# Kernel optimization log

Measured on AMD Instinct MI355X. Metric: run time of the kernel, lower is better.

Reference implementation:

```python
import jax, jax.numpy as jnp
import numpy as np

N_QUBITS = 12
N_LAYERS = 4
BATCH = 4096
DIM = 2 ** N_QUBITS  # 4096


def _apply_1q(state, U, q):
    """Apply 2x2 complex gate U to qubit q. state: (B,) + (2,)*n, wire 0 = MSB (axis q+1)."""
    state = jnp.moveaxis(state, q + 1, -1)
    state = state @ U.T
    return jnp.moveaxis(state, -1, q + 1)


def _apply_cnot(state, c, t):
    """CNOT with control c, target t: flip target amplitudes where control bit == 1."""
    flipped = jnp.flip(state, axis=t + 1)
    shape = [2 if i == c + 1 else 1 for i in range(state.ndim)]
    ctrl = jnp.arange(2).reshape(shape)
    return jnp.where(ctrl == 1, flipped, state)


def setup_inputs() -> dict:
    key = jax.random.key(0)
    k1, k2 = jax.random.split(key)
    x = jax.random.normal(k1, (BATCH, DIM), dtype=jnp.float32)
    weights = jax.random.normal(k2, (N_LAYERS, N_QUBITS, 2), dtype=jnp.float32) * 0.1
    return {"x": x, "weights": weights}


def reference(x, weights):
    n, L = N_QUBITS, N_LAYERS
    B = x.shape[0]
    # AmplitudeEmbedding with normalize=True
    norm = jnp.linalg.norm(x, axis=-1, keepdims=True)
    state = (x / norm).astype(jnp.complex64).reshape((B,) + (2,) * n)
    for layer in range(L):
        for q in range(n):
            ty = weights[layer, q, 0]
            tz = weights[layer, q, 1]
            c, s = jnp.cos(ty / 2), jnp.sin(ty / 2)
            em = jnp.exp(-0.5j * tz.astype(jnp.complex64))  # e^{-i tz/2}
            ep = jnp.exp(+0.5j * tz.astype(jnp.complex64))
            # U = RZ(tz) @ RY(ty), fused single 2x2 gate per qubit
            U = jnp.stack([
                jnp.stack([c * em, -s * em]),
                jnp.stack([s * ep, c * ep]),
            ]).astype(jnp.complex64)
            state = _apply_1q(state, U, q)
        for q in range(n - 1):
            state = _apply_cnot(state, q, q + 1)
        if n > 2:
            state = _apply_cnot(state, n - 1, 0)
    probs = jnp.abs(state) ** 2  # (B,) + (2,)*n, float32
    reduce_axes = tuple(range(1, probs.ndim))
    outs = []
    for q in range(n):
        shape = [2 if i == q + 1 else 1 for i in range(probs.ndim)]
        sign = jnp.array([1.0, -1.0], dtype=probs.dtype).reshape(shape)
        outs.append(jnp.sum(probs * sign, axis=reduce_axes))
    return jnp.stack(outs, axis=-1)  # (B, n_qubits) <Z_q> expvals
```

## Files before the change

### kernel.cpp

```cpp
#include <hip/hip_runtime.h>

#define NQ   12
#define DIM  4096
#define NL   4
#define BLK  256

typedef unsigned short u16;
typedef unsigned int   u32;
typedef float f2 __attribute__((ext_vector_type(2)));

struct L12 { u16 b[NQ]; };

static constexpr u32 lap(const L12& A, u32 x){ u32 r=0; for(int p=0;p<NQ;++p) if((x>>p)&1u) r^=A.b[p]; return r; }
static constexpr L12 lcomp(const L12& A, const L12& B){ L12 r{}; for(int p=0;p<NQ;++p) r.b[p]=(u16)lap(A,(u32)B.b[p]); return r; }
static constexpr L12 lident(){ L12 r{}; for(int p=0;p<NQ;++p) r.b[p]=(u16)(1u<<p); return r; }

static constexpr u32 applyT(u32 i){
  i ^= ((i>>0)&1u) << 11;
  for(int q=10;q>=0;--q){ int pc=11-q, pt=10-q; i ^= ((i>>pc)&1u) << pt; }
  return i;
}
static constexpr L12 lT(){ L12 t{}; for(int p=0;p<NQ;++p) t.b[p]=(u16)applyT(1u<<p); return t; }

static constexpr L12 linv(const L12& A){
  u16 v[NQ]; u16 u[NQ];
  for(int p=0;p<NQ;++p){ v[p]=A.b[p]; u[p]=(u16)(1u<<p); }
  for(int t=0;t<NQ;++t){
    int p=t; while(!((v[p]>>t)&1u)) ++p;
    u16 tv=v[p]; v[p]=v[t]; v[t]=tv; u16 tu=u[p]; u[p]=u[t]; u[t]=tu;
    for(int k=0;k<NQ;++k) if(k!=t && ((v[k]>>t)&1u)){ v[k]^=v[t]; u[k]^=u[t]; }
  }
  L12 r{}; for(int p=0;p<NQ;++p) r.b[p]=u[p]; return r;
}
static constexpr L12 ltr(const L12& A){
  L12 r{}; for(int p=0;p<NQ;++p) for(int q=0;q<NQ;++q) if((A.b[p]>>q)&1u) r.b[q]=(u16)(r.b[q]|(1u<<p));
  return r;
}
static constexpr int cpop(u32 v){ int n=0; while(v){ n+=(int)(v&1u); v>>=1; } return n; }

struct Tables {
  u16 cm[12][16];
  u16 wg[12][4];
  u16 sp[12][4];
  u16 wexp[NQ];
};

static constexpr Tables make_tables(){
  Tables tb{};
  const L12 T   = lT();
  const L12 Tit = ltr(linv(T));
  L12 A = lident();
  L12 W = lident();
  for(int l=0;l<NL;++l){
    for(int g=0;g<3;++g){
      const int st = l*3+g;
      u16 mm[4]={0,0,0,0};
      for(int i=0;i<4;++i){ mm[i]=A.b[4*g+i]; tb.wg[st][i]=W.b[4*g+i]; }
      u32 ech[4]={0,0,0,0}; int piv[4]={0,0,0,0};
      for(int i=0;i<4;++i){
        u32 v=mm[i];
        for(int k=0;k<i;++k) if((v>>piv[k])&1u) v^=ech[k];
        int t2=11; while(!((v>>t2)&1u)) --t2;
        piv[i]=t2; ech[i]=v;
      }
      for(int a2=0;a2<4;++a2) for(int b2=a2+1;b2<4;++b2)
        if(piv[b2]<piv[a2]){ int tt=piv[a2]; piv[a2]=piv[b2]; piv[b2]=tt; }
      for(int i=0;i<4;++i) tb.sp[st][i]=(u16)piv[i];
      for(int c=0;c<16;++c){ u32 m=0; for(int i=0;i<4;++i) if((c>>i)&1) m^=mm[i]; tb.cm[st][c]=(u16)m; }
    }
    A = lcomp(A, T);
    W = lcomp(W, Tit);
  }
  for(int p=0;p<NQ;++p) tb.wexp[p]=W.b[p];
  return tb;
}

__device__ constexpr Tables TB = make_tables();

static constexpr u16 UIMG[12] = {1,2,4,8, 3,5,6,7, 9,10,11,13};

static constexpr u32 swz(u32 j){
  u32 f=0;
  for(int k=4;k<12;++k) if((j>>k)&1u) f ^= (u32)UIMG[k];
  return j ^ (f & 15u);
}

struct Derived {
  u32 lane_c[12][8];
  u32 smb[12][4];
  u32 scmb[12][16];
  u32 g0lane[8];
  u32 u11lane[8];
  u32 u11smb[4];
  u16 pm[12];
  u16 mu[12];
};

static constexpr Derived make_derived(){
  const Tables tb = make_tables();
  Derived d{};
  for(int st=0; st<12; ++st){
    bool isp[12]={false,false,false,false,false,false,false,false,false,false,false,false};
    for(int i=0;i<4;++i) isp[tb.sp[st][i]]=true;
    int np[8]; int nn=0;
    for(int p=0;p<12;++p) if(!isp[p]) np[nn++]=p;
    int best=-1;
    for(int ms=0; ms<256; ++ms){
      int pc=0; for(int k=0;k<8;++k) pc+=(ms>>k)&1;
      if(pc!=6) continue;
      u16 bas[4]={0,0,0,0}; int r=0;
      for(int k=0;k<8;++k){
        if(!((ms>>k)&1)) continue;
        u16 x=(u16)(UIMG[np[k]]&15);
        while(x){
          int hb=3; while(!((x>>hb)&1)) --hb;
          if(bas[hb]) x=(u16)(x^bas[hb]);
          else { bas[hb]=x; ++r; x=0; }
        }
      }
      if(r==4){ best=ms; break; }
    }
    if(best<0) best=0x3F;
    int pos[8]; int lo=0, hi=6;
    for(int k=0;k<8;++k){ if((best>>k)&1) pos[lo++]=np[k]; else pos[hi++]=np[k]; }
    for(int k=0;k<8;++k){
      const u32 addr = swz(1u<<pos[k])<<3;
      u32 nib=0;
      for(int i=0;i<4;++i) nib |= (u32)((tb.wg[st][i]>>pos[k])&1u)<<i;
      d.lane_c[st][k] = addr | (nib<<28);
      if(st==0)  d.g0lane[k]  = 1u<<pos[k];
      if(st==11) d.u11lane[k] = 1u<<pos[k];
    }
    for(int i=0;i<4;++i)  d.smb[st][i]  = swz((u32)tb.cm[st][1<<i])<<3;
    for(int c=0;c<16;++c) d.scmb[st][c] = swz((u32)tb.cm[st][c])<<3;
    if(st==11) for(int i=0;i<4;++i) d.u11smb[i] = (u32)tb.cm[11][1<<i];
  }
  for(int q=0;q<12;++q){
    d.pm[q] = tb.wexp[11-q];
    u32 m=0;
    for(int i=0;i<4;++i) m |= (u32)(cpop((u32)tb.cm[11][1u<<i] & (u32)tb.wexp[11-q])&1)<<i;
    d.mu[q]=(u16)m;
  }
  return d;
}

__device__ constexpr Derived DV = make_derived();

template<int ST, bool WITHW>
__device__ __forceinline__ void gates(f2 (&a)[16], const float4* __restrict__ gw){
#pragma unroll
  for(int i=0;i<4;++i){
    const float4 g = gw[ST*4+i];
    const f2 mt = {-g.x, -g.x};
    const f2 sy = { g.y,  g.y};
#pragma unroll
    for(int c=0;c<16;++c){
      if((c>>i)&1) continue;
      const int c1 = c|(1<<i);
      f2 u = __builtin_elementwise_fma(mt, a[c1], a[c]);
      f2 v = __builtin_elementwise_fma(sy, u, a[c1]);
      a[c] = __builtin_elementwise_fma(mt, v, u);
      if(WITHW){
        const float t = fmaf(-g.z, v.y, v.x);
        v.y = fmaf( g.w, t, v.y);
        v.x = fmaf(-g.z, v.y, t);
      }
      a[c1]=v;
    }
  }
}

template<int ST, bool WITHW>
__device__ __forceinline__ void mid_step(const u32* msk, char* lds, const float4* __restrict__ gw){
  u32 acc=0;
#pragma unroll
  for(int k=0;k<8;++k) acc ^= DV.lane_c[ST][k]&msk[k];
  const u32 nib = acc>>28;
  u32 base = acc & 0x0FFFFFFFu;
#pragma unroll
  for(int i=0;i<4;++i) base ^= DV.smb[ST][i] & (0u-((nib>>i)&1u));
  u32 ad[16]; f2 a[16];
#pragma unroll
  for(int c=0;c<16;++c){
    ad[c] = base ^ DV.scmb[ST][c];
    a[c] = *(const f2*)(lds+ad[c]);
  }
  gates<ST,WITHW>(a,gw);
#pragma unroll
  for(int c=0;c<16;++c){ *(f2*)(lds+ad[c]) = a[c]; }
  __syncthreads();
}

__global__ void prep_kernel(const float* __restrict__ w, float4* __restrict__ gw){
  const int t = threadIdx.x;
  if(t < NL*NQ){
    const int l=t/NQ, p=t%NQ, q=(NQ-1)-p;
    const float ty=w[(l*NQ+q)*2+0], tz=w[(l*NQ+q)*2+1];
    gw[t]=make_float4(tanf(0.25f*ty), sinf(0.5f*ty), tanf(0.5f*tz), sinf(tz));
  }
}

__global__ __launch_bounds__(BLK, 5) void qsim_kernel(const float* __restrict__ x,
                                                      const float4* __restrict__ gw,
                                                      float* __restrict__ out)
{
  __shared__ f2 st2[DIM];
  char* lds = (char*)st2;
  const int tid = threadIdx.x;
  const int bb  = blockIdx.x;

  u32 msk[8];
#pragma unroll
  for(int k=0;k<8;++k) msk[k]=0u-((u32)(tid>>k)&1u);

  u32 rep0=0, acc0=0;
#pragma unroll
  for(int k=0;k<8;++k){ rep0 ^= DV.g0lane[k]&msk[k]; acc0 ^= DV.lane_c[0][k]&msk[k]; }
  const u32 base0 = acc0 & 0x0FFFFFFFu;

  f2 a[16];
  const float* xr = x + (size_t)bb*DIM + rep0;
#pragma unroll
  for(int s=0;s<4;++s){
    const float4 v = *reinterpret_cast<const float4*>(xr + 4*s);
    a[4*s+0]=(f2){v.x,0.f}; a[4*s+1]=(f2){v.y,0.f};
    a[4*s+2]=(f2){v.z,0.f}; a[4*s+3]=(f2){v.w,0.f};
  }
  gates<0,true>(a,gw);
#pragma unroll
  for(int c=0;c<16;++c){ *(f2*)(lds + (base0 ^ DV.scmb[0][c])) = a[c]; }
  __syncthreads();

  mid_step<1,true >(msk,lds,gw);
  mid_step<2,true >(msk,lds,gw);
  mid_step<3,true >(msk,lds,gw);
  mid_step<4,true >(msk,lds,gw);
  mid_step<5,true >(msk,lds,gw);
  mid_step<6,true >(msk,lds,gw);
  mid_step<7,true >(msk,lds,gw);
  mid_step<8,true >(msk,lds,gw);
  mid_step<9,false>(msk,lds,gw);
  mid_step<10,false>(msk,lds,gw);

  {
    u32 acc=0, urep=0;
#pragma unroll
    for(int k=0;k<8;++k){ acc ^= DV.lane_c[11][k]&msk[k]; urep ^= DV.u11lane[k]&msk[k]; }
    const u32 nib = acc>>28;
    u32 base = acc & 0x0FFFFFFFu;
#pragma unroll
    for(int i=0;i<4;++i){ const u32 mi=0u-((nib>>i)&1u); base ^= DV.smb[11][i]&mi; urep ^= DV.u11smb[i]&mi; }
#pragma unroll
    for(int c=0;c<16;++c){
      a[c] = *(const f2*)(lds + (base ^ DV.scmb[11][c]));
    }
    gates<11,false>(a,gw);

    float pr[16];
#pragma unroll
    for(int c=0;c<16;++c) pr[c]=fmaf(a[c].x,a[c].x, a[c].y*a[c].y);
#pragma unroll
    for(int b=1;b<16;b<<=1){
#pragma unroll
      for(int c=0;c<16;++c){
        if(c&b) continue;
        const float u=pr[c], v=pr[c|b];
        pr[c]=u+v; pr[c|b]=u-v;
      }
    }
    float accq[12];
#pragma unroll
    for(int q=0;q<12;++q){
      const u32 sb = ((u32)__popc(urep & (u32)DV.pm[q]) & 1u)<<31;
      accq[q]=__uint_as_float(__float_as_uint(pr[DV.mu[q]])^sb);
    }
    float nrm2 = pr[0];
#pragma unroll
    for(int o=32;o;o>>=1){
      nrm2 += __shfl_xor(nrm2,o);
#pragma unroll
      for(int q=0;q<12;++q) accq[q]+=__shfl_xor(accq[q],o);
    }
    __syncthreads();
    float* wredf = (float*)lds;
    const int wid=tid>>6;
    if((tid&63)==0){
#pragma unroll
      for(int q=0;q<12;++q) wredf[wid*13+q]=accq[q];
      wredf[wid*13+12]=nrm2;
    }
    __syncthreads();
    if(tid<NQ){
      const float s0=wredf[0*13+tid]+wredf[1*13+tid]+wredf[2*13+tid]+wredf[3*13+tid];
      const float sn=wredf[0*13+12]+wredf[1*13+12]+wredf[2*13+12]+wredf[3*13+12];
      out[(size_t)bb*NQ+tid]=s0/sn;
    }
  }
}

extern "C" void kernel_launch(void* const* d_in, const int* in_sizes, int n_in,
                              void* d_out, int out_size, void* d_ws, size_t ws_size,
                              hipStream_t stream) {
  const float* x = (const float*)d_in[0];
  const float* w = (const float*)d_in[1];
  float* out = (float*)d_out;
  float4* gw = (float4*)d_ws;
  const int B = in_sizes[0] / DIM;
  prep_kernel<<<1, 64, 0, stream>>>(w, gw);
  qsim_kernel<<<B, BLK, 0, stream>>>(x, gw, out);
}
```

Measured before the change: 107.0 us.

## Process two batch rows per block with split real/imag packed-FMA layout

Each block now simulates two batch samples at once, storing amplitudes as (re0,re1,im0,im1) float4 in LDS so v_pk_fma_f32 runs on the same component of both samples. This changes the gate arithmetic from mixed real/imag pairs to fully packed operations, doubles the LDS footprint per block, and rebuilds the swizzle/bank selection search for 16-byte entries. Occupancy hint drops from 5 to 2 blocks, and half as many blocks are launched. The aim is to use packed FP32 throughput fully and halve per-sample index/sync overhead, at the cost of more registers and LDS per block.

```diff
diff --git a/kernel.cpp b/kernel.cpp
--- a/kernel.cpp
+++ b/kernel.cpp
@@ -8,6 +8,7 @@
 typedef unsigned short u16;
 typedef unsigned int   u32;
 typedef float f2 __attribute__((ext_vector_type(2)));
+typedef float f4v __attribute__((ext_vector_type(4)));
 
 struct L12 { u16 b[NQ]; };
 
@@ -75,14 +76,24 @@
   return tb;
 }
 
-__device__ constexpr Tables TB = make_tables();
-
 static constexpr u16 UIMG[12] = {1,2,4,8, 3,5,6,7, 9,10,11,13};
 
 static constexpr u32 swz(u32 j){
   u32 f=0;
   for(int k=4;k<12;++k) if((j>>k)&1u) f ^= (u32)UIMG[k];
   return j ^ (f & 15u);
+}
+
+static constexpr int rankbits(const u16* v, int n, u16 mask){
+  u16 bas[4]={0,0,0,0}; int r=0;
+  for(int i=0;i<n;++i){
+    u16 x=(u16)(v[i]&mask);
+    for(int it=0; it<5 && x; ++it){
+      int hb=3; while(hb>0 && !((x>>hb)&1u)) --hb;
+      if(bas[hb]) x=(u16)(x^bas[hb]); else { bas[hb]=x; ++r; x=0; }
+    }
+  }
+  return r;
 }
 
 struct Derived {
@@ -104,35 +115,40 @@
     for(int i=0;i<4;++i) isp[tb.sp[st][i]]=true;
     int np[8]; int nn=0;
     for(int p=0;p<12;++p) if(!isp[p]) np[nn++]=p;
-    int best=-1;
-    for(int ms=0; ms<256; ++ms){
-      int pc=0; for(int k=0;k<8;++k) pc+=(ms>>k)&1;
-      if(pc!=6) continue;
-      u16 bas[4]={0,0,0,0}; int r=0;
-      for(int k=0;k<8;++k){
-        if(!((ms>>k)&1)) continue;
-        u16 x=(u16)(UIMG[np[k]]&15);
-        while(x){
-          int hb=3; while(!((x>>hb)&1)) --hb;
-          if(bas[hb]) x=(u16)(x^bas[hb]);
-          else { bas[hb]=x; ++r; x=0; }
+    u16 img8[8];
+    for(int j=0;j<8;++j) img8[j]=(u16)(swz(1u<<np[j])&15u);
+    int ord[8]={0,1,2,3,4,5,6,7}; bool okf=false;
+    for(int a=0;a<8&&!okf;++a)for(int b=a+1;b<8&&!okf;++b)
+    for(int c2=b+1;c2<8&&!okf;++c2)for(int dd=c2+1;dd<8&&!okf;++dd){
+      u16 four[4]={img8[a],img8[b],img8[c2],img8[dd]};
+      if(rankbits(four,4,15)!=4) continue;
+      const int ids[4]={a,b,c2,dd};
+      for(int ex=0; ex<4 && !okf; ++ex){
+        u16 tri[3]; int tj=0;
+        for(int j=0;j<4;++j) if(j!=ex) tri[tj++]=four[j];
+        if(rankbits(tri,3,7)!=3) continue;
+        int pp=0;
+        for(int j=0;j<4;++j) if(j!=ex) ord[pp++]=ids[j];
+        ord[3]=ids[ex];
+        int rp=4;
+        for(int j=0;j<8;++j){
+          bool used=false; for(int k2=0;k2<4;++k2) if(ids[k2]==j) used=true;
+          if(!used) ord[rp++]=j;
         }
-      }
-      if(r==4){ best=ms; break; }
-    }
-    if(best<0) best=0x3F;
-    int pos[8]; int lo=0, hi=6;
-    for(int k=0;k<8;++k){ if((best>>k)&1) pos[lo++]=np[k]; else pos[hi++]=np[k]; }
+        okf=true;
+      }
+    }
     for(int k=0;k<8;++k){
-      const u32 addr = swz(1u<<pos[k])<<3;
+      const int pos = np[ord[k]];
+      const u32 addr = swz(1u<<pos)<<4;
       u32 nib=0;
-      for(int i=0;i<4;++i) nib |= (u32)((tb.wg[st][i]>>pos[k])&1u)<<i;
+      for(int i=0;i<4;++i) nib |= (u32)((tb.wg[st][i]>>pos)&1u)<<i;
       d.lane_c[st][k] = addr | (nib<<28);
-      if(st==0)  d.g0lane[k]  = 1u<<pos[k];
-      if(st==11) d.u11lane[k] = 1u<<pos[k];
-    }
-    for(int i=0;i<4;++i)  d.smb[st][i]  = swz((u32)tb.cm[st][1<<i])<<3;
-    for(int c=0;c<16;++c) d.scmb[st][c] = swz((u32)tb.cm[st][c])<<3;
+      if(st==0)  d.g0lane[k]  = 1u<<pos;
+      if(st==11) d.u11lane[k] = 1u<<pos;
+    }
+    for(int i=0;i<4;++i)  d.smb[st][i]  = swz((u32)tb.cm[st][1<<i])<<4;
+    for(int c=0;c<16;++c) d.scmb[st][c] = swz((u32)tb.cm[st][c])<<4;
     if(st==11) for(int i=0;i<4;++i) d.u11smb[i] = (u32)tb.cm[11][1<<i];
   }
   for(int q=0;q<12;++q){
@@ -146,26 +162,37 @@
 
 __device__ constexpr Derived DV = make_derived();
 
+__device__ __forceinline__ f2 pkfma(f2 a, f2 b, f2 c){
+  f2 d;
+  asm("v_pk_fma_f32 %0, %1, %2, %3" : "=v"(d) : "v"(a), "v"(b), "v"(c));
+  return d;
+}
+
 template<int ST, bool WITHW>
-__device__ __forceinline__ void gates(f2 (&a)[16], const float4* __restrict__ gw){
+__device__ __forceinline__ void gates(f2 (&R)[16], f2 (&I)[16], const float4* __restrict__ gw){
 #pragma unroll
   for(int i=0;i<4;++i){
     const float4 g = gw[ST*4+i];
-    const f2 mt = {-g.x, -g.x};
-    const f2 sy = { g.y,  g.y};
+    const f2 mt  = {g.x, g.x};
+    const f2 sy  = {g.y, g.y};
+    const f2 mgz = {g.z, g.z};
+    const f2 sw  = {g.w, g.w};
 #pragma unroll
     for(int c=0;c<16;++c){
       if((c>>i)&1) continue;
       const int c1 = c|(1<<i);
-      f2 u = __builtin_elementwise_fma(mt, a[c1], a[c]);
-      f2 v = __builtin_elementwise_fma(sy, u, a[c1]);
-      a[c] = __builtin_elementwise_fma(mt, v, u);
+      f2 uR = pkfma(mt, R[c1], R[c]);
+      f2 uI = pkfma(mt, I[c1], I[c]);
+      f2 vR = pkfma(sy, uR, R[c1]);
+      f2 vI = pkfma(sy, uI, I[c1]);
+      R[c] = pkfma(mt, vR, uR);
+      I[c] = pkfma(mt, vI, uI);
       if(WITHW){
-        const float t = fmaf(-g.z, v.y, v.x);
-        v.y = fmaf( g.w, t, v.y);
-        v.x = fmaf(-g.z, v.y, t);
-      }
-      a[c1]=v;
+        const f2 tr = pkfma(mgz, vI, vR);
+        vI = pkfma(sw, tr, vI);
+        vR = pkfma(mgz, vI, tr);
+      }
+      R[c1]=vR; I[c1]=vI;
     }
   }
 }
@@ -179,15 +206,16 @@
   u32 base = acc & 0x0FFFFFFFu;
 #pragma unroll
   for(int i=0;i<4;++i) base ^= DV.smb[ST][i] & (0u-((nib>>i)&1u));
-  u32 ad[16]; f2 a[16];
+  u32 ad[16]; f2 R[16], I[16];
 #pragma unroll
   for(int c=0;c<16;++c){
     ad[c] = base ^ DV.scmb[ST][c];
-    a[c] = *(const f2*)(lds+ad[c]);
-  }
-  gates<ST,WITHW>(a,gw);
-#pragma unroll
-  for(int c=0;c<16;++c){ *(f2*)(lds+ad[c]) = a[c]; }
+    const f4v v = *(const f4v*)(lds+ad[c]);
+    R[c]=v.lo; I[c]=v.hi;
+  }
+  gates<ST,WITHW>(R,I,gw);
+#pragma unroll
+  for(int c=0;c<16;++c){ f4v v; v.lo=R[c]; v.hi=I[c]; *(f4v*)(lds+ad[c]) = v; }
   __syncthreads();
 }
 
@@ -196,16 +224,16 @@
   if(t < NL*NQ){
     const int l=t/NQ, p=t%NQ, q=(NQ-1)-p;
     const float ty=w[(l*NQ+q)*2+0], tz=w[(l*NQ+q)*2+1];
-    gw[t]=make_float4(tanf(0.25f*ty), sinf(0.5f*ty), tanf(0.5f*tz), sinf(tz));
-  }
-}
-
-__global__ __launch_bounds__(BLK, 5) void qsim_kernel(const float* __restrict__ x,
+    gw[t]=make_float4(-tanf(0.25f*ty), sinf(0.5f*ty), -tanf(0.5f*tz), sinf(tz));
+  }
+}
+
+__global__ __launch_bounds__(BLK, 2) void qsim_kernel(const float* __restrict__ x,
                                                       const float4* __restrict__ gw,
                                                       float* __restrict__ out)
 {
-  __shared__ f2 st2[DIM];
-  char* lds = (char*)st2;
+  __shared__ f4v st4[DIM];
+  char* lds = (char*)st4;
   const int tid = threadIdx.x;
   const int bb  = blockIdx.x;
 
@@ -218,17 +246,22 @@
   for(int k=0;k<8;++k){ rep0 ^= DV.g0lane[k]&msk[k]; acc0 ^= DV.lane_c[0][k]&msk[k]; }
   const u32 base0 = acc0 & 0x0FFFFFFFu;
 
-  f2 a[16];
-  const float* xr = x + (size_t)bb*DIM + rep0;
+  f2 R[16], I[16];
+  const float* xr0 = x + (size_t)(2*bb)*DIM + rep0;
+  const float* xr1 = xr0 + DIM;
 #pragma unroll
   for(int s=0;s<4;++s){
-    const float4 v = *reinterpret_cast<const float4*>(xr + 4*s);
-    a[4*s+0]=(f2){v.x,0.f}; a[4*s+1]=(f2){v.y,0.f};
-    a[4*s+2]=(f2){v.z,0.f}; a[4*s+3]=(f2){v.w,0.f};
-  }
-  gates<0,true>(a,gw);
-#pragma unroll
-  for(int c=0;c<16;++c){ *(f2*)(lds + (base0 ^ DV.scmb[0][c])) = a[c]; }
+    const float4 v0 = *reinterpret_cast<const float4*>(xr0 + 4*s);
+    const float4 v1 = *reinterpret_cast<const float4*>(xr1 + 4*s);
+    R[4*s+0]=(f2){v0.x,v1.x}; R[4*s+1]=(f2){v0.y,v1.y};
+    R[4*s+2]=(f2){v0.z,v1.z}; R[4*s+3]=(f2){v0.w,v1.w};
+    I[4*s+0]=(f2){0.f,0.f};   I[4*s+1]=(f2){0.f,0.f};
+    I[4*s+2]=(f2){0.f,0.f};   I[4*s+3]=(f2){0.f,0.f};
+  }
+  gates<0,true>(R,I,gw);
+#pragma unroll
+  for(int c=0;c<16;++c){ f4v v; v.lo=R[c]; v.hi=I[c];
+    *(f4v*)(lds + (base0 ^ DV.scmb[0][c])) = v; }
   __syncthreads();
 
   mid_step<1,true >(msk,lds,gw);
@@ -252,48 +285,58 @@
     for(int i=0;i<4;++i){ const u32 mi=0u-((nib>>i)&1u); base ^= DV.smb[11][i]&mi; urep ^= DV.u11smb[i]&mi; }
 #pragma unroll
     for(int c=0;c<16;++c){
-      a[c] = *(const f2*)(lds + (base ^ DV.scmb[11][c]));
-    }
-    gates<11,false>(a,gw);
-
-    float pr[16];
-#pragma unroll
-    for(int c=0;c<16;++c) pr[c]=fmaf(a[c].x,a[c].x, a[c].y*a[c].y);
+      const f4v v = *(const f4v*)(lds + (base ^ DV.scmb[11][c]));
+      R[c]=v.lo; I[c]=v.hi;
+    }
+    gates<11,false>(R,I,gw);
+
+    f2 pr[16];
+#pragma unroll
+    for(int c=0;c<16;++c) pr[c]=pkfma(R[c],R[c], pkfma(I[c],I[c],(f2){0.f,0.f}));
+    const f2 mone = {-1.f,-1.f};
 #pragma unroll
     for(int b=1;b<16;b<<=1){
 #pragma unroll
       for(int c=0;c<16;++c){
         if(c&b) continue;
-        const float u=pr[c], v=pr[c|b];
-        pr[c]=u+v; pr[c|b]=u-v;
-      }
-    }
-    float accq[12];
+        const f2 u=pr[c], v=pr[c|b];
+        pr[c]=u+v;
+        pr[c|b]=pkfma(v,mone,u);
+      }
+    }
+    f2 accq[12];
 #pragma unroll
     for(int q=0;q<12;++q){
       const u32 sb = ((u32)__popc(urep & (u32)DV.pm[q]) & 1u)<<31;
-      accq[q]=__uint_as_float(__float_as_uint(pr[DV.mu[q]])^sb);
-    }
-    float nrm2 = pr[0];
+      const f2 a = pr[DV.mu[q]];
+      accq[q]=(f2){__uint_as_float(__float_as_uint(a.x)^sb),
+                   __uint_as_float(__float_as_uint(a.y)^sb)};
+    }
+    f2 nrm2 = pr[0];
 #pragma unroll
     for(int o=32;o;o>>=1){
-      nrm2 += __shfl_xor(nrm2,o);
-#pragma unroll
-      for(int q=0;q<12;++q) accq[q]+=__shfl_xor(accq[q],o);
+      nrm2.x += __shfl_xor(nrm2.x,o);
+      nrm2.y += __shfl_xor(nrm2.y,o);
+#pragma unroll
+      for(int q=0;q<12;++q){
+        accq[q].x += __shfl_xor(accq[q].x,o);
+        accq[q].y += __shfl_xor(accq[q].y,o);
+      }
     }
     __syncthreads();
-    float* wredf = (float*)lds;
+    f2* wredp = (f2*)lds;
     const int wid=tid>>6;
     if((tid&63)==0){
 #pragma unroll
-      for(int q=0;q<12;++q) wredf[wid*13+q]=accq[q];
-      wredf[wid*13+12]=nrm2;
+      for(int q=0;q<12;++q) wredp[wid*13+q]=accq[q];
+      wredp[wid*13+12]=nrm2;
     }
     __syncthreads();
     if(tid<NQ){
-      const float s0=wredf[0*13+tid]+wredf[1*13+tid]+wredf[2*13+tid]+wredf[3*13+tid];
-      const float sn=wredf[0*13+12]+wredf[1*13+12]+wredf[2*13+12]+wredf[3*13+12];
-      out[(size_t)bb*NQ+tid]=s0/sn;
+      const f2 s0=wredp[0*13+tid]+wredp[1*13+tid]+wredp[2*13+tid]+wredp[3*13+tid];
+      const f2 sn=wredp[0*13+12]+wredp[1*13+12]+wredp[2*13+12]+wredp[3*13+12];
+      out[(size_t)(2*bb+0)*NQ+tid]=s0.x/sn.x;
+      out[(size_t)(2*bb+1)*NQ+tid]=s0.y/sn.y;
     }
   }
 }
@@ -307,5 +350,5 @@
   float4* gw = (float4*)d_ws;
   const int B = in_sizes[0] / DIM;
   prep_kernel<<<1, 64, 0, stream>>>(w, gw);
-  qsim_kernel<<<B, BLK, 0, stream>>>(x, gw, out);
-}
+  qsim_kernel<<<B/2, BLK, 0, stream>>>(x, gw, out);
+}
```

New measurement: 114.9 us. 7.3% more time.

## Pair gate stages into thread-private LDS groups to halve block barriers

Applied to the files above, without the earlier changes.

Adds compile-time GF(2) linear-algebra search that, for each pair of consecutive gate stages, finds a lane assignment where every thread's second-stage amplitudes were all written by that same thread in the first stage. A cheap s_waitcnt then replaces the block-wide __syncthreads between them, roughly halving the number of barriers. It also unvectorizes the gate FMAs into scalar fmaf calls and lowers the launch_bounds occupancy hint from 5 to 4. The fallback path runs if the constexpr search fails, and correctness depends on the per-thread disjointness proof being right.

```diff
diff --git a/kernel.cpp b/kernel.cpp
--- a/kernel.cpp
+++ b/kernel.cpp
@@ -9,6 +9,10 @@
 typedef unsigned int   u32;
 typedef float f2 __attribute__((ext_vector_type(2)));
 
+static constexpr int pcnt(u32 v){ return __builtin_popcount(v); }
+static constexpr int par(u32 v){ return pcnt(v)&1; }
+static constexpr int hb(u16 v){ for(int i=11;i>=0;--i) if((v>>i)&1u) return i; return -1; }
+
 struct L12 { u16 b[NQ]; };
 
 static constexpr u32 lap(const L12& A, u32 x){ u32 r=0; for(int p=0;p<NQ;++p) if((x>>p)&1u) r^=A.b[p]; return r; }
@@ -17,13 +21,13 @@
 
 static constexpr u32 applyT(u32 i){
   i ^= ((i>>0)&1u) << 11;
-  for(int q=10;q>=0;--q){ int pc=11-q, pt=10-q; i ^= ((i>>pc)&1u) << pt; }
+  for(int q=10;q>=0;--q){ int pc2=11-q, pt=10-q; i ^= ((i>>pc2)&1u) << pt; }
   return i;
 }
 static constexpr L12 lT(){ L12 t{}; for(int p=0;p<NQ;++p) t.b[p]=(u16)applyT(1u<<p); return t; }
 
 static constexpr L12 linv(const L12& A){
-  u16 v[NQ]; u16 u[NQ];
+  u16 v[NQ]={}; u16 u[NQ]={};
   for(int p=0;p<NQ;++p){ v[p]=A.b[p]; u[p]=(u16)(1u<<p); }
   for(int t=0;t<NQ;++t){
     int p=t; while(!((v[p]>>t)&1u)) ++p;
@@ -36,7 +40,6 @@
   L12 r{}; for(int p=0;p<NQ;++p) for(int q=0;q<NQ;++q) if((A.b[p]>>q)&1u) r.b[q]=(u16)(r.b[q]|(1u<<p));
   return r;
 }
-static constexpr int cpop(u32 v){ int n=0; while(v){ n+=(int)(v&1u); v>>=1; } return n; }
 
 struct Tables {
   u16 cm[12][16];
@@ -75,14 +78,47 @@
   return tb;
 }
 
-__device__ constexpr Tables TB = make_tables();
-
 static constexpr u16 UIMG[12] = {1,2,4,8, 3,5,6,7, 9,10,11,13};
 
 static constexpr u32 swz(u32 j){
   u32 f=0;
   for(int k=4;k<12;++k) if((j>>k)&1u) f ^= (u32)UIMG[k];
   return j ^ (f & 15u);
+}
+
+struct Ech { u16 s[12]; };
+static constexpr u16 ered(const Ech& e, u16 x){
+  while(x){
+    const int lb=hb(x);
+    if(e.s[lb]) x=(u16)(x^e.s[lb]); else break;
+  }
+  return x;
+}
+static constexpr bool eadd(Ech& e, u16 x){
+  x=ered(e,x); if(!x) return false;
+  e.s[hb(x)]=x; return true;
+}
+
+struct NullB { u16 v[12]; int n; };
+static constexpr NullB nullspace(const u16* rows, int m){
+  u16 rr[12]={}; int pcl[12]={}; int nr=0;
+  for(int i=0;i<m;++i){
+    u16 x=rows[i];
+    for(int j=0;j<nr;++j) if((x>>pcl[j])&1u) x=(u16)(x^rr[j]);
+    if(!x) continue;
+    const int lb=hb(x);
+    for(int j=0;j<nr;++j) if((rr[j]>>lb)&1u) rr[j]=(u16)(rr[j]^x);
+    rr[nr]=x; pcl[nr]=lb; ++nr;
+  }
+  NullB nb{};
+  for(int f=0;f<12;++f){
+    bool isp=false; for(int j=0;j<nr;++j) if(pcl[j]==f) isp=true;
+    if(isp) continue;
+    u16 x=(u16)(1u<<f);
+    for(int j=0;j<nr;++j) if((rr[j]>>f)&1u) x=(u16)(x|(1u<<pcl[j]));
+    nb.v[nb.n++]=x;
+  }
+  return nb;
 }
 
 struct Derived {
@@ -100,28 +136,27 @@
   const Tables tb = make_tables();
   Derived d{};
   for(int st=0; st<12; ++st){
-    bool isp[12]={false,false,false,false,false,false,false,false,false,false,false,false};
+    bool isp[12]={};
     for(int i=0;i<4;++i) isp[tb.sp[st][i]]=true;
-    int np[8]; int nn=0;
+    int np[8]={}; int nn=0;
     for(int p=0;p<12;++p) if(!isp[p]) np[nn++]=p;
     int best=-1;
     for(int ms=0; ms<256; ++ms){
-      int pc=0; for(int k=0;k<8;++k) pc+=(ms>>k)&1;
-      if(pc!=6) continue;
+      if(pcnt((u32)ms)!=6) continue;
       u16 bas[4]={0,0,0,0}; int r=0;
       for(int k=0;k<8;++k){
         if(!((ms>>k)&1)) continue;
         u16 x=(u16)(UIMG[np[k]]&15);
         while(x){
-          int hb=3; while(!((x>>hb)&1)) --hb;
-          if(bas[hb]) x=(u16)(x^bas[hb]);
-          else { bas[hb]=x; ++r; x=0; }
+          int hbx=3; while(!((x>>hbx)&1)) --hbx;
+          if(bas[hbx]) x=(u16)(x^bas[hbx]);
+          else { bas[hbx]=x; ++r; x=0; }
         }
       }
       if(r==4){ best=ms; break; }
     }
     if(best<0) best=0x3F;
-    int pos[8]; int lo=0, hi=6;
+    int pos[8]={}; int lo=0, hi=6;
     for(int k=0;k<8;++k){ if((best>>k)&1) pos[lo++]=np[k]; else pos[hi++]=np[k]; }
     for(int k=0;k<8;++k){
       const u32 addr = swz(1u<<pos[k])<<3;
@@ -138,28 +173,162 @@
   for(int q=0;q<12;++q){
     d.pm[q] = tb.wexp[11-q];
     u32 m=0;
-    for(int i=0;i<4;++i) m |= (u32)(cpop((u32)tb.cm[11][1u<<i] & (u32)tb.wexp[11-q])&1)<<i;
+    for(int i=0;i<4;++i) m |= (u32)(par((u32)tb.cm[11][1u<<i] & (u32)tb.wexp[11-q]))<<i;
     d.mu[q]=(u16)m;
   }
   return d;
 }
 
 __device__ constexpr Derived DV = make_derived();
+
+struct Pair2 {
+  u32 lane_c[8];
+  u32 smbA[4], smbB[4];
+  u32 sA[16], sB[16];
+  u32 rawlane[8], rawA[4], rawB[4];
+  bool ok;
+};
+
+static constexpr bool cand_ok(u16 x, bool lowc, const Ech& eA, const Ech& eB,
+                              const Ech& bank, bool needbank){
+  if(!x) return false;
+  if(lowc && (x&15u)) return false;
+  if(!ered(eA,x)) return false;
+  if(!ered(eB,x)) return false;
+  if(needbank){ const u16 img=(u16)(swz(x)&15u); if(!img) return false; if(!ered(bank,img)) return false; }
+  return true;
+}
+
+static constexpr Pair2 make_pair2(int a, int att){
+  Pair2 r{};
+  const Tables tb = make_tables();
+  const int b=a+1;
+  u16 A[4]={}, B[4]={}, rows[8]={};
+  for(int i=0;i<4;++i){ A[i]=tb.cm[a][1u<<i]; B[i]=tb.cm[b][1u<<i]; rows[i]=A[i]; rows[4+i]=B[i]; }
+  const NullB ann = nullspace(rows,8);
+  if(ann.n<2) return r;
+  const u16 f6=ann.v[0], f7=ann.v[1];
+  const bool lowc = (a==0);
+  u16 u6=0,u7=0;
+  for(u32 j=1;j<4096u && !(u6&&u7);++j){
+    const u16 x = lowc ? (u16)((j&255u)<<4) : (u16)j;
+    if(lowc && j>255u) break;
+    if(!x) continue;
+    const int s6=par((u32)(x&f6)), s7=par((u32)(x&f7));
+    if(!u6 && s6==1 && s7==0) u6=x;
+    else if(!u7 && s6==0 && s7==1) u7=x;
+  }
+  if(!u6||!u7) return r;
+  u16 fr[2]={f6,f7};
+  const NullB K = nullspace(fr,2);
+  u16 W[6]={};
+  Ech eA{}; for(int i=0;i<4;++i) eadd(eA,A[i]);
+  Ech eB{}; for(int i=0;i<4;++i) eadd(eB,B[i]);
+  Ech bank{};
+  for(int k=0;k<6;++k){
+    u16 pick=0;
+    for(int pref=1; pref>=0 && !pick; --pref){
+      const bool nb = (k<4) && (pref==1);
+      int skip = att;
+      for(int i1=0;i1<K.n && !pick;++i1){
+        const u16 x=K.v[i1];
+        if(cand_ok(x,lowc,eA,eB,bank,nb)){ if(skip){--skip;} else pick=x; }
+      }
+      for(int i1=0;i1<K.n && !pick;++i1)
+        for(int j1=i1+1;j1<K.n && !pick;++j1){
+          const u16 x=(u16)(K.v[i1]^K.v[j1]);
+          if(cand_ok(x,lowc,eA,eB,bank,nb)){ if(skip){--skip;} else pick=x; }
+        }
+      for(int i1=0;i1<4 && !pick;++i1)
+        for(int j1=i1+1;j1<K.n && !pick;++j1)
+          for(int l1=j1+1;l1<K.n && !pick;++l1){
+            const u16 x=(u16)(K.v[i1]^K.v[j1]^K.v[l1]);
+            if(cand_ok(x,lowc,eA,eB,bank,nb)){ if(skip){--skip;} else pick=x; }
+          }
+    }
+    if(!pick) return r;
+    W[k]=pick; eadd(eA,pick); eadd(eB,pick);
+    if(k<4){ const u16 img=(u16)(swz(pick)&15u); if(img) eadd(bank,img); }
+  }
+  const u16 vv[8] = {W[0],W[1],W[2],W[3],W[4],W[5],u6,u7};
+  u16 beta[4]={};
+  for(int j=0;j<4;++j){
+    u16 m=0;
+    for(int i=0;i<4;++i) m|=(u16)(par((u32)(A[j]&tb.wg[b][i]))<<i);
+    beta[j]=m;
+  }
+  for(int k=0;k<8;++k){
+    const u16 v=vv[k];
+    u32 nibA=0, nibB=0;
+    for(int i=0;i<4;++i) nibA|=(u32)par((u32)(v&tb.wg[a][i]))<<i;
+    for(int i=0;i<4;++i) nibB|=(u32)par((u32)(v&tb.wg[b][i]))<<i;
+    for(int j=0;j<4;++j) if((nibA>>j)&1u) nibB^=(u32)beta[j];
+    r.lane_c[k]=(swz((u32)v)<<3)|(nibB<<24)|(nibA<<28);
+    r.rawlane[k]=(u32)v;
+  }
+  for(int i=0;i<4;++i){
+    r.smbA[i]=swz((u32)A[i])<<3; r.smbB[i]=swz((u32)B[i])<<3;
+    r.rawA[i]=(u32)A[i];         r.rawB[i]=(u32)B[i];
+  }
+  for(int c=0;c<16;++c){ r.sA[c]=swz((u32)tb.cm[a][c])<<3; r.sB[c]=swz((u32)tb.cm[b][c])<<3; }
+  u16 gens[8]={};
+  for(int k=0;k<8;++k){
+    const u32 nibA=(r.lane_c[k]>>28)&15u;
+    u16 g=vv[k];
+    for(int j=0;j<4;++j) if((nibA>>j)&1u) g=(u16)(g^A[j]);
+    gens[k]=g;
+  }
+  {
+    Ech e{}; int rk=0;
+    for(int k=0;k<8;++k) if(eadd(e,gens[k])) ++rk;
+    for(int i=0;i<4;++i) if(eadd(e,B[i])) ++rk;
+    if(rk!=12) return r;
+  }
+  {
+    Ech e{}; int rk=0;
+    for(int k=0;k<8;++k) if(eadd(e,gens[k])) ++rk;
+    for(int i=0;i<4;++i) if(eadd(e,A[i])) ++rk;
+    if(rk!=12) return r;
+  }
+  if(lowc){ for(int k=0;k<8;++k) if(vv[k]&15u) return r; }
+  r.ok=true;
+  return r;
+}
+
+static constexpr Pair2 mkpair(int a){
+  {
+    const Pair2 p = make_pair2(a,0);
+    if(p.ok) return p;
+  }
+  {
+    const Pair2 p = make_pair2(a,1);
+    if(p.ok) return p;
+  }
+  Pair2 bad{}; bad.ok=false; return bad;
+}
+
+static constexpr Pair2 P0h = mkpair(0);
+static constexpr Pair2 P1h = mkpair(2);
+static constexpr Pair2 P2h = mkpair(4);
+static constexpr Pair2 P3h = mkpair(6);
+static constexpr Pair2 P4h = mkpair(8);
+static constexpr Pair2 P5h = mkpair(10);
+
+__device__ constexpr Pair2 PAIRS[6] = {P0h,P1h,P2h,P3h,P4h,P5h};
 
 template<int ST, bool WITHW>
 __device__ __forceinline__ void gates(f2 (&a)[16], const float4* __restrict__ gw){
 #pragma unroll
   for(int i=0;i<4;++i){
     const float4 g = gw[ST*4+i];
-    const f2 mt = {-g.x, -g.x};
-    const f2 sy = { g.y,  g.y};
 #pragma unroll
     for(int c=0;c<16;++c){
       if((c>>i)&1) continue;
       const int c1 = c|(1<<i);
-      f2 u = __builtin_elementwise_fma(mt, a[c1], a[c]);
-      f2 v = __builtin_elementwise_fma(sy, u, a[c1]);
-      a[c] = __builtin_elementwise_fma(mt, v, u);
+      f2 u, v;
+      u.x = fmaf(-g.x, a[c1].x, a[c].x);  u.y = fmaf(-g.x, a[c1].y, a[c].y);
+      v.x = fmaf( g.y, u.x, a[c1].x);     v.y = fmaf( g.y, u.y, a[c1].y);
+      a[c].x = fmaf(-g.x, v.x, u.x);      a[c].y = fmaf(-g.x, v.y, u.y);
       if(WITHW){
         const float t = fmaf(-g.z, v.y, v.x);
         v.y = fmaf( g.w, t, v.y);
@@ -191,16 +360,52 @@
   __syncthreads();
 }
 
-__global__ void prep_kernel(const float* __restrict__ w, float4* __restrict__ gw){
+__device__ __forceinline__ void ds_fence(){
+  asm volatile("s_waitcnt lgkmcnt(0)" ::: "memory");
+}
+
+template<int PI, int SA, bool WA, bool WB>
+__device__ __forceinline__ void pair_mid(const u32* msk, char* lds, const float4* __restrict__ gw){
+  if constexpr (PAIRS[PI].ok){
+    u32 acc=0;
+#pragma unroll
+    for(int k=0;k<8;++k) acc ^= PAIRS[PI].lane_c[k]&msk[k];
+    const u32 nibA=(acc>>28)&15u, nibB=(acc>>24)&15u;
+    u32 baseA = acc & 0x00FFFFFFu;
+#pragma unroll
+    for(int i=0;i<4;++i) baseA ^= PAIRS[PI].smbA[i] & (0u-((nibA>>i)&1u));
+    u32 ad[16]; f2 a[16];
+#pragma unroll
+    for(int c=0;c<16;++c){ ad[c]=baseA ^ PAIRS[PI].sA[c]; a[c]=*(const f2*)(lds+ad[c]); }
+    gates<SA,WA>(a,gw);
+#pragma unroll
+    for(int c=0;c<16;++c){ *(f2*)(lds+ad[c]) = a[c]; }
+    ds_fence();
+    u32 baseB = baseA;
+#pragma unroll
+    for(int i=0;i<4;++i) baseB ^= PAIRS[PI].smbB[i] & (0u-((nibB>>i)&1u));
+#pragma unroll
+    for(int c=0;c<16;++c){ ad[c]=baseB ^ PAIRS[PI].sB[c]; a[c]=*(const f2*)(lds+ad[c]); }
+    gates<SA+1,WB>(a,gw);
+#pragma unroll
+    for(int c=0;c<16;++c){ *(f2*)(lds+ad[c]) = a[c]; }
+    __syncthreads();
+  } else {
+    mid_step<SA,WA>(msk,lds,gw);
+    mid_step<SA+1,WB>(msk,lds,gw);
+  }
+}
+
+__global__ void prep_kernel(const float* __restrict__ w, float4* __restrict__ gwS){
   const int t = threadIdx.x;
   if(t < NL*NQ){
     const int l=t/NQ, p=t%NQ, q=(NQ-1)-p;
     const float ty=w[(l*NQ+q)*2+0], tz=w[(l*NQ+q)*2+1];
-    gw[t]=make_float4(tanf(0.25f*ty), sinf(0.5f*ty), tanf(0.5f*tz), sinf(tz));
-  }
-}
-
-__global__ __launch_bounds__(BLK, 5) void qsim_kernel(const float* __restrict__ x,
+    gwS[t]=make_float4(tanf(0.25f*ty), sinf(0.5f*ty), tanf(0.5f*tz), sinf(tz));
+  }
+}
+
+__global__ __launch_bounds__(BLK, 4) void qsim_kernel(const float* __restrict__ x,
                                                       const float4* __restrict__ gw,
                                                       float* __restrict__ out)
 {
@@ -213,37 +418,86 @@
 #pragma unroll
   for(int k=0;k<8;++k) msk[k]=0u-((u32)(tid>>k)&1u);
 
-  u32 rep0=0, acc0=0;
-#pragma unroll
-  for(int k=0;k<8;++k){ rep0 ^= DV.g0lane[k]&msk[k]; acc0 ^= DV.lane_c[0][k]&msk[k]; }
-  const u32 base0 = acc0 & 0x0FFFFFFFu;
-
-  f2 a[16];
-  const float* xr = x + (size_t)bb*DIM + rep0;
-#pragma unroll
-  for(int s=0;s<4;++s){
-    const float4 v = *reinterpret_cast<const float4*>(xr + 4*s);
-    a[4*s+0]=(f2){v.x,0.f}; a[4*s+1]=(f2){v.y,0.f};
-    a[4*s+2]=(f2){v.z,0.f}; a[4*s+3]=(f2){v.w,0.f};
-  }
-  gates<0,true>(a,gw);
-#pragma unroll
-  for(int c=0;c<16;++c){ *(f2*)(lds + (base0 ^ DV.scmb[0][c])) = a[c]; }
-  __syncthreads();
-
-  mid_step<1,true >(msk,lds,gw);
-  mid_step<2,true >(msk,lds,gw);
-  mid_step<3,true >(msk,lds,gw);
-  mid_step<4,true >(msk,lds,gw);
-  mid_step<5,true >(msk,lds,gw);
-  mid_step<6,true >(msk,lds,gw);
-  mid_step<7,true >(msk,lds,gw);
-  mid_step<8,true >(msk,lds,gw);
-  mid_step<9,false>(msk,lds,gw);
-  mid_step<10,false>(msk,lds,gw);
-
-  {
-    u32 acc=0, urep=0;
+  if constexpr (PAIRS[0].ok){
+    u32 acc=0, rep0=0;
+#pragma unroll
+    for(int k=0;k<8;++k){ acc ^= PAIRS[0].lane_c[k]&msk[k]; rep0 ^= PAIRS[0].rawlane[k]&msk[k]; }
+    const u32 nibA=(acc>>28)&15u, nibB=(acc>>24)&15u;
+    u32 baseA = acc & 0x00FFFFFFu;
+#pragma unroll
+    for(int i=0;i<4;++i){ const u32 mi=0u-((nibA>>i)&1u); baseA ^= PAIRS[0].smbA[i]&mi; rep0 ^= PAIRS[0].rawA[i]&mi; }
+    f2 a[16];
+    const float* xr = x + (size_t)bb*DIM + rep0;
+#pragma unroll
+    for(int s=0;s<4;++s){
+      const float4 v = *reinterpret_cast<const float4*>(xr + 4*s);
+      a[4*s+0]=(f2){v.x,0.f}; a[4*s+1]=(f2){v.y,0.f};
+      a[4*s+2]=(f2){v.z,0.f}; a[4*s+3]=(f2){v.w,0.f};
+    }
+    gates<0,true>(a,gw);
+#pragma unroll
+    for(int c=0;c<16;++c){ *(f2*)(lds + (baseA ^ PAIRS[0].sA[c])) = a[c]; }
+    ds_fence();
+    u32 baseB = baseA;
+#pragma unroll
+    for(int i=0;i<4;++i) baseB ^= PAIRS[0].smbB[i] & (0u-((nibB>>i)&1u));
+    u32 ad[16];
+#pragma unroll
+    for(int c=0;c<16;++c){ ad[c]=baseB ^ PAIRS[0].sB[c]; a[c]=*(const f2*)(lds+ad[c]); }
+    gates<1,true>(a,gw);
+#pragma unroll
+    for(int c=0;c<16;++c){ *(f2*)(lds+ad[c]) = a[c]; }
+    __syncthreads();
+  } else {
+    u32 rep0=0, acc0=0;
+#pragma unroll
+    for(int k=0;k<8;++k){ rep0 ^= DV.g0lane[k]&msk[k]; acc0 ^= DV.lane_c[0][k]&msk[k]; }
+    const u32 base0 = acc0 & 0x0FFFFFFFu;
+    f2 a[16];
+    const float* xr = x + (size_t)bb*DIM + rep0;
+#pragma unroll
+    for(int s=0;s<4;++s){
+      const float4 v = *reinterpret_cast<const float4*>(xr + 4*s);
+      a[4*s+0]=(f2){v.x,0.f}; a[4*s+1]=(f2){v.y,0.f};
+      a[4*s+2]=(f2){v.z,0.f}; a[4*s+3]=(f2){v.w,0.f};
+    }
+    gates<0,true>(a,gw);
+#pragma unroll
+    for(int c=0;c<16;++c){ *(f2*)(lds + (base0 ^ DV.scmb[0][c])) = a[c]; }
+    __syncthreads();
+    mid_step<1,true>(msk,lds,gw);
+  }
+
+  pair_mid<1,2,true,true >(msk,lds,gw);
+  pair_mid<2,4,true,true >(msk,lds,gw);
+  pair_mid<3,6,true,true >(msk,lds,gw);
+  pair_mid<4,8,true,false>(msk,lds,gw);
+
+  f2 a[16]; u32 urep=0;
+  if constexpr (PAIRS[5].ok){
+    u32 acc=0;
+#pragma unroll
+    for(int k=0;k<8;++k){ acc ^= PAIRS[5].lane_c[k]&msk[k]; urep ^= PAIRS[5].rawlane[k]&msk[k]; }
+    const u32 nibA=(acc>>28)&15u, nibB=(acc>>24)&15u;
+    u32 baseA = acc & 0x00FFFFFFu;
+#pragma unroll
+    for(int i=0;i<4;++i){ const u32 mi=0u-((nibA>>i)&1u); baseA ^= PAIRS[5].smbA[i]&mi; urep ^= PAIRS[5].rawA[i]&mi; }
+    u32 ad[16];
+#pragma unroll
+    for(int c=0;c<16;++c){ ad[c]=baseA ^ PAIRS[5].sA[c]; a[c]=*(const f2*)(lds+ad[c]); }
+    gates<10,false>(a,gw);
+#pragma unroll
+    for(int c=0;c<16;++c){ *(f2*)(lds+ad[c]) = a[c]; }
+    ds_fence();
+    u32 baseB = baseA;
+#pragma unroll
+    for(int i=0;i<4;++i){ const u32 mi=0u-((nibB>>i)&1u); baseB ^= PAIRS[5].smbB[i]&mi; urep ^= PAIRS[5].rawB[i]&mi; }
+#pragma unroll
+    for(int c=0;c<16;++c){ a[c]=*(const f2*)(lds + (baseB ^ PAIRS[5].sB[c])); }
+    gates<11,false>(a,gw);
+  } else {
+    mid_step<10,false>(msk,lds,gw);
+    u32 acc=0;
 #pragma unroll
     for(int k=0;k<8;++k){ acc ^= DV.lane_c[11][k]&msk[k]; urep ^= DV.u11lane[k]&msk[k]; }
     const u32 nib = acc>>28;
@@ -251,11 +505,11 @@
 #pragma unroll
     for(int i=0;i<4;++i){ const u32 mi=0u-((nib>>i)&1u); base ^= DV.smb[11][i]&mi; urep ^= DV.u11smb[i]&mi; }
 #pragma unroll
-    for(int c=0;c<16;++c){
-      a[c] = *(const f2*)(lds + (base ^ DV.scmb[11][c]));
-    }
+    for(int c=0;c<16;++c){ a[c] = *(const f2*)(lds + (base ^ DV.scmb[11][c])); }
     gates<11,false>(a,gw);
-
+  }
+
+  {
     float pr[16];
 #pragma unroll
     for(int c=0;c<16;++c) pr[c]=fmaf(a[c].x,a[c].x, a[c].y*a[c].y);
@@ -304,8 +558,8 @@
   const float* x = (const float*)d_in[0];
   const float* w = (const float*)d_in[1];
   float* out = (float*)d_out;
-  float4* gw = (float4*)d_ws;
+  float4* gwS = (float4*)d_ws;
   const int B = in_sizes[0] / DIM;
-  prep_kernel<<<1, 64, 0, stream>>>(w, gw);
-  qsim_kernel<<<B, BLK, 0, stream>>>(x, gw, out);
-}
+  prep_kernel<<<1, 64, 0, stream>>>(w, gwS);
+  qsim_kernel<<<B, BLK, 0, stream>>>(x, gwS, out);
+}
```

Result: slower. 109.4 us (+2.3%).
